# Performance work log

Hardware: AMD Instinct MI355X
Metric: run time of the kernel (lower is better)

Reference implementation:

```python
import jax, jax.numpy as jnp
import numpy as np

B, N_IN, L, W, N_OUT, D = 4096, 1024, 8, 1024, 1024, 16
W_SCALE = 0.25  # 1/sqrt(fan_in) so tanh does not saturate


def setup_inputs() -> dict:
    key = jax.random.key(0)
    ks = jax.random.split(key, 5)
    x = jax.random.normal(ks[0], (B, N_IN), dtype=jnp.float32)
    # each hidden-layer node gathers D values from the previous layer
    src_hidden = jax.random.randint(ks[1], (L, W, D), 0, N_IN, dtype=jnp.int32)
    w_hidden = jax.random.normal(ks[2], (L, W, D), dtype=jnp.float32) * W_SCALE
    src_out = jax.random.randint(ks[3], (N_OUT, D), 0, W, dtype=jnp.int32)
    w_out = jax.random.normal(ks[4], (N_OUT, D), dtype=jnp.float32) * W_SCALE
    return {"x": x, "src_hidden": src_hidden, "w_hidden": w_hidden,
            "src_out": src_out, "w_out": w_out}


def reference(x, src_hidden, w_hidden, src_out, w_out):
    # Topological-order evaluation, one fused gather-weighted-sum-activation
    # per layer instead of the original per-node Python loop.
    def layer(vals, sw):
        src, w = sw                                   # [W, D] each
        # vals[:, src]: [B, W, D] gather; weighted incoming sum then tanh
        new_vals = jnp.tanh(jnp.sum(vals[:, src] * w, axis=-1))  # [B, W]
        return new_vals, None

    vals, _ = jax.lax.scan(layer, x, (src_hidden, w_hidden))
    # output nodes: identity activation (weighted sum only)
    out = jnp.sum(vals[:, src_out] * w_out, axis=-1)   # [B, N_OUT]
    return out
```

## Files before the change

kernel.cpp:

```cpp
#include <hip/hip_runtime.h>


#define TB       8
#define W_NODES  1024
#define LAYERS   8
#define ROW_H    8
#define BUF_H    (W_NODES * ROW_H)

typedef _Float16 h8 __attribute__((ext_vector_type(8)));

__device__ __forceinline__ float fast_tanh(float x) {
    float a = __builtin_amdgcn_exp2f(x * 2.8853900817779268f);
    return 1.0f - 2.0f * __builtin_amdgcn_rcpf(a + 1.0f);
}

__device__ __forceinline__ void gather16(const _Float16* __restrict__ rd,
                                         const int* __restrict__ si,
                                         const float* __restrict__ wi,
                                         float* __restrict__ acc)
{
#define LDV(i) (*(const h8*)(rd + (si[i] << 3)))
#define FMA8(g, w)                                        \
    do {                                                  \
        const float _w = (w);                             \
        _Pragma("unroll")                                 \
        for (int j = 0; j < TB; ++j)                      \
            acc[j] = fmaf((float)(g)[j], _w, acc[j]);     \
    } while (0)

    h8 g0 = LDV(0);  h8 g1 = LDV(1);  h8 g2 = LDV(2);  h8 g3 = LDV(3);
    h8 g4 = LDV(4);  h8 g5 = LDV(5);  h8 g6 = LDV(6);  h8 g7 = LDV(7);

    FMA8(g0, wi[0]);  FMA8(g1, wi[1]);
    g0 = LDV(8);      g1 = LDV(9);
    FMA8(g2, wi[2]);  FMA8(g3, wi[3]);
    g2 = LDV(10);     g3 = LDV(11);
    FMA8(g4, wi[4]);  FMA8(g5, wi[5]);
    g4 = LDV(12);     g5 = LDV(13);
    FMA8(g6, wi[6]);  FMA8(g7, wi[7]);
    g6 = LDV(14);     g7 = LDV(15);

    FMA8(g0, wi[8]);  FMA8(g1, wi[9]);
    FMA8(g2, wi[10]); FMA8(g3, wi[11]);
    FMA8(g4, wi[12]); FMA8(g5, wi[13]);
    FMA8(g6, wi[14]); FMA8(g7, wi[15]);
#undef LDV
#undef FMA8
}

__global__ __launch_bounds__(1024, 8) void genome_net(
    const float* __restrict__ x,
    const int*   __restrict__ src_hidden,
    const float* __restrict__ w_hidden,
    const int*   __restrict__ src_out,
    const float* __restrict__ w_out,
    float*       __restrict__ out)
{
    extern __shared__ _Float16 lds[];
    _Float16* bufA = lds;
    _Float16* bufB = lds + BUF_H;

    const int t  = threadIdx.x;
    const int b0 = blockIdx.x * TB;

    {
        h8 hv;
        #pragma unroll
        for (int j = 0; j < TB; ++j)
            hv[j] = (_Float16)x[(size_t)(b0 + j) * W_NODES + t];
        *(h8*)(bufA + t * ROW_H) = hv;
    }
    __syncthreads();

    _Float16* rd = bufA;
    _Float16* wr = bufB;

    #pragma unroll 1
    for (int l = 0; l < LAYERS; ++l) {
        const int row = (l << 10) + t;
        const int4*   sp = (const int4*)(src_hidden) + (row << 2);
        const float4* wp = (const float4*)(w_hidden) + (row << 2);
        int4   s4[4]; float4 w4[4];
        #pragma unroll
        for (int q = 0; q < 4; ++q) { s4[q] = sp[q]; w4[q] = wp[q]; }
        int   si[16]; float wi[16];
        #pragma unroll
        for (int q = 0; q < 4; ++q) {
            si[4*q+0] = s4[q].x; si[4*q+1] = s4[q].y;
            si[4*q+2] = s4[q].z; si[4*q+3] = s4[q].w;
            wi[4*q+0] = w4[q].x; wi[4*q+1] = w4[q].y;
            wi[4*q+2] = w4[q].z; wi[4*q+3] = w4[q].w;
        }

        float acc[TB];
        #pragma unroll
        for (int j = 0; j < TB; ++j) acc[j] = 0.0f;

        gather16(rd, si, wi, acc);

        h8 hv;
        #pragma unroll
        for (int j = 0; j < TB; ++j) hv[j] = (_Float16)fast_tanh(acc[j]);
        *(h8*)(wr + t * ROW_H) = hv;

        __syncthreads();
        _Float16* tmp = rd; rd = wr; wr = tmp;
    }

    {
        const int4*   sp = (const int4*)(src_out) + (t << 2);
        const float4* wp = (const float4*)(w_out) + (t << 2);
        int4   s4[4]; float4 w4[4];
        #pragma unroll
        for (int q = 0; q < 4; ++q) { s4[q] = sp[q]; w4[q] = wp[q]; }
        int   si[16]; float wi[16];
        #pragma unroll
        for (int q = 0; q < 4; ++q) {
            si[4*q+0] = s4[q].x; si[4*q+1] = s4[q].y;
            si[4*q+2] = s4[q].z; si[4*q+3] = s4[q].w;
            wi[4*q+0] = w4[q].x; wi[4*q+1] = w4[q].y;
            wi[4*q+2] = w4[q].z; wi[4*q+3] = w4[q].w;
        }

        float acc[TB];
        #pragma unroll
        for (int j = 0; j < TB; ++j) acc[j] = 0.0f;

        gather16(rd, si, wi, acc);

        #pragma unroll
        for (int j = 0; j < TB; ++j)
            out[(size_t)(b0 + j) * W_NODES + t] = acc[j];
    }
}

extern "C" void kernel_launch(void* const* d_in, const int* in_sizes, int n_in,
                              void* d_out, int out_size, void* d_ws, size_t ws_size,
                              hipStream_t stream) {
    const float* x  = (const float*)d_in[0];
    const int*   sh = (const int*)  d_in[1];
    const float* wh = (const float*)d_in[2];
    const int*   so = (const int*)  d_in[3];
    const float* wo = (const float*)d_in[4];
    float* out = (float*)d_out;

    const int shmem = 2 * BUF_H * (int)sizeof(_Float16);
    hipFuncSetAttribute(reinterpret_cast<const void*>(genome_net),
                        hipFuncAttributeMaxDynamicSharedMemorySize, shmem);

    genome_net<<<dim3(4096 / TB), dim3(1024), shmem, stream>>>(
        x, sh, wh, so, wo, out);
}
```

Baseline: 113.3 us.

## Process 16 batch rows per block with thread pairs splitting each node's row

The per-block batch tile is doubled from 8 to 16 rows, so each LDS row now holds 16 fp16 values per node. Each thread handles two nodes and one 8-wide half of the batch, with pairs of adjacent threads sharing a node. This halves the block count and the number of times src/weight rows are read per batch element. In exchange, LDS per block doubles to 64 KB and occupancy drops to 4 waves per SIMD. Adjacent lanes now touch neighbouring 16-byte halves of the same gathered row, which may change LDS bank-conflict behaviour.

Result: faster. 110.6 us, median of 2 (-2.4%).

```diff
diff --git a/kernel.cpp b/kernel.cpp
--- a/kernel.cpp
+++ b/kernel.cpp
@@ -1,10 +1,10 @@
 #include <hip/hip_runtime.h>
 
 
-#define TB       8
+#define TB       16
 #define W_NODES  1024
 #define LAYERS   8
-#define ROW_H    8
+#define ROW_H    16
 #define BUF_H    (W_NODES * ROW_H)
 
 typedef _Float16 h8 __attribute__((ext_vector_type(8)));
@@ -14,17 +14,18 @@
     return 1.0f - 2.0f * __builtin_amdgcn_rcpf(a + 1.0f);
 }
 
-__device__ __forceinline__ void gather16(const _Float16* __restrict__ rd,
-                                         const int* __restrict__ si,
-                                         const float* __restrict__ wi,
-                                         float* __restrict__ acc)
+__device__ __forceinline__ void gather16_half(const _Float16* __restrict__ rd,
+                                              const int* __restrict__ si,
+                                              const float* __restrict__ wi,
+                                              const int hfo,
+                                              float* __restrict__ acc)
 {
-#define LDV(i) (*(const h8*)(rd + (si[i] << 3)))
+#define LDV(i) (*(const h8*)(rd + ((si[i] << 4) + hfo)))
 #define FMA8(g, w)                                        \
     do {                                                  \
         const float _w = (w);                             \
         _Pragma("unroll")                                 \
-        for (int j = 0; j < TB; ++j)                      \
+        for (int j = 0; j < 8; ++j)                       \
             acc[j] = fmaf((float)(g)[j], _w, acc[j]);     \
     } while (0)
 
@@ -48,7 +49,7 @@
 #undef FMA8
 }
 
-__global__ __launch_bounds__(1024, 8) void genome_net(
+__global__ __launch_bounds__(1024, 4) void genome_net(
     const float* __restrict__ x,
     const int*   __restrict__ src_hidden,
     const float* __restrict__ w_hidden,
@@ -60,15 +61,21 @@
     _Float16* bufA = lds;
     _Float16* bufB = lds + BUF_H;
 
-    const int t  = threadIdx.x;
-    const int b0 = blockIdx.x * TB;
+    const int t   = threadIdx.x;
+    const int pr  = t >> 1;
+    const int hf  = t & 1;
+    const int hfo = hf << 3;
+    const int b0  = blockIdx.x * TB;
+    const int bb  = b0 + hfo;
 
-    {
+    #pragma unroll
+    for (int p = 0; p < 2; ++p) {
+        const int n = (p << 9) + pr;
         h8 hv;
         #pragma unroll
-        for (int j = 0; j < TB; ++j)
-            hv[j] = (_Float16)x[(size_t)(b0 + j) * W_NODES + t];
-        *(h8*)(bufA + t * ROW_H) = hv;
+        for (int j = 0; j < 8; ++j)
+            hv[j] = (_Float16)x[(size_t)(bb + j) * W_NODES + n];
+        *(h8*)(bufA + n * ROW_H + hfo) = hv;
     }
     __syncthreads();
 
@@ -77,9 +84,45 @@
 
     #pragma unroll 1
     for (int l = 0; l < LAYERS; ++l) {
-        const int row = (l << 10) + t;
-        const int4*   sp = (const int4*)(src_hidden) + (row << 2);
-        const float4* wp = (const float4*)(w_hidden) + (row << 2);
+        #pragma unroll
+        for (int p = 0; p < 2; ++p) {
+            const int n   = (p << 9) + pr;
+            const int row = (l << 10) + n;
+            const int4*   sp = (const int4*)(src_hidden) + (row << 2);
+            const float4* wp = (const float4*)(w_hidden) + (row << 2);
+            int4   s4[4]; float4 w4[4];
+            #pragma unroll
+            for (int q = 0; q < 4; ++q) { s4[q] = sp[q]; w4[q] = wp[q]; }
+            int   si[16]; float wi[16];
+            #pragma unroll
+            for (int q = 0; q < 4; ++q) {
+                si[4*q+0] = s4[q].x; si[4*q+1] = s4[q].y;
+                si[4*q+2] = s4[q].z; si[4*q+3] = s4[q].w;
+                wi[4*q+0] = w4[q].x; wi[4*q+1] = w4[q].y;
+                wi[4*q+2] = w4[q].z; wi[4*q+3] = w4[q].w;
+            }
+
+            float acc[8];
+            #pragma unroll
+            for (int j = 0; j < 8; ++j) acc[j] = 0.0f;
+
+            gather16_half(rd, si, wi, hfo, acc);
+
+            h8 hv;
+            #pragma unroll
+            for (int j = 0; j < 8; ++j) hv[j] = (_Float16)fast_tanh(acc[j]);
+            *(h8*)(wr + n * ROW_H + hfo) = hv;
+        }
+
+        __syncthreads();
+        _Float16* tmp = rd; rd = wr; wr = tmp;
+    }
+
+    #pragma unroll
+    for (int p = 0; p < 2; ++p) {
+        const int n = (p << 9) + pr;
+        const int4*   sp = (const int4*)(src_out) + (n << 2);
+        const float4* wp = (const float4*)(w_out) + (n << 2);
         int4   s4[4]; float4 w4[4];
         #pragma unroll
         for (int q = 0; q < 4; ++q) { s4[q] = sp[q]; w4[q] = wp[q]; }
@@ -92,45 +135,15 @@
             wi[4*q+2] = w4[q].z; wi[4*q+3] = w4[q].w;
         }
 
-        float acc[TB];
+        float acc[8];
         #pragma unroll
-        for (int j = 0; j < TB; ++j) acc[j] = 0.0f;
+        for (int j = 0; j < 8; ++j) acc[j] = 0.0f;
 
-        gather16(rd, si, wi, acc);
-
-        h8 hv;
-        #pragma unroll
-        for (int j = 0; j < TB; ++j) hv[j] = (_Float16)fast_tanh(acc[j]);
-        *(h8*)(wr + t * ROW_H) = hv;
-
-        __syncthreads();
-        _Float16* tmp = rd; rd = wr; wr = tmp;
-    }
-
-    {
-        const int4*   sp = (const int4*)(src_out) + (t << 2);
-        const float4* wp = (const float4*)(w_out) + (t << 2);
-        int4   s4[4]; float4 w4[4];
-        #pragma unroll
-        for (int q = 0; q < 4; ++q) { s4[q] = sp[q]; w4[q] = wp[q]; }
-        int   si[16]; float wi[16];
-        #pragma unroll
-        for (int q = 0; q < 4; ++q) {
-            si[4*q+0] = s4[q].x; si[4*q+1] = s4[q].y;
-            si[4*q+2] = s4[q].z; si[4*q+3] = s4[q].w;
-            wi[4*q+0] = w4[q].x; wi[4*q+1] = w4[q].y;
-            wi[4*q+2] = w4[q].z; wi[4*q+3] = w4[q].w;
-        }
-
-        float acc[TB];
-        #pragma unroll
-        for (int j = 0; j < TB; ++j) acc[j] = 0.0f;
-
-        gather16(rd, si, wi, acc);
+        gather16_half(rd, si, wi, hfo, acc);
 
         #pragma unroll
-        for (int j = 0; j < TB; ++j)
-            out[(size_t)(b0 + j) * W_NODES + t] = acc[j];
+        for (int j = 0; j < 8; ++j)
+            out[(size_t)(bb + j) * W_NODES + n] = acc[j];
     }
 }
 
```
